# Kernel tuning notes

Measured on AMD Instinct MI355X. Metric: run time of the kernel, lower is better.

The kernel has to match this reference:

```python
import jax, jax.numpy as jnp
import numpy as np

B, C, H, W = 32, 3, 224, 224
P = 16
D = 768
HEADS, DH = 12, 64
INNER = HEADS * DH          # 768
DEPTH = 12
NUM_CLASSES = 1000
NP_ = (H // P) * (W // P)   # 196 patches
N = NP_ + 1                 # with cls token
PATCH_DIM = C * P * P       # 768
EPS = 1e-5


def _ln(x, g, b):
    mu = jnp.mean(x, axis=-1, keepdims=True)
    var = jnp.var(x, axis=-1, keepdims=True)
    return (x - mu) * jax.lax.rsqrt(var + EPS) * g + b


def setup_inputs() -> dict:
    key = jax.random.key(0)
    ks = jax.random.split(key, 16)
    s = 0.02
    return {
        "img": jax.random.normal(ks[0], (B, C, H, W), jnp.float32),
        "sph_dist": jax.random.uniform(ks[1], (N, N), jnp.float32),
        "patch_ln_g": jnp.ones((PATCH_DIM,), jnp.float32),
        "patch_ln_b": jnp.zeros((PATCH_DIM,), jnp.float32),
        "W_patch": jax.random.normal(ks[2], (PATCH_DIM, D), jnp.float32) * s,
        "b_patch": jnp.zeros((D,), jnp.float32),
        "emb_ln_g": jnp.ones((D,), jnp.float32),
        "emb_ln_b": jnp.zeros((D,), jnp.float32),
        "pos_emb": jax.random.normal(ks[3], (1, N, D), jnp.float32),
        "cls_tok": jax.random.normal(ks[4], (1, 1, D), jnp.float32),
        "ln_g": jnp.ones((DEPTH, D), jnp.float32),
        "ln_b": jnp.zeros((DEPTH, D), jnp.float32),
        "W_qkv": jax.random.normal(ks[5], (DEPTH, D, 3 * INNER), jnp.float32) * s,
        "W_out": jax.random.normal(ks[6], (DEPTH, INNER, D), jnp.float32) * s,
        "b_out": jnp.zeros((DEPTH, D), jnp.float32),
        "final_ln_g": jnp.ones((D,), jnp.float32),
        "final_ln_b": jnp.zeros((D,), jnp.float32),
        "W_head": jax.random.normal(ks[7], (D, NUM_CLASSES), jnp.float32) * s,
        "b_head": jnp.zeros((NUM_CLASSES,), jnp.float32),
    }


def _patchify(img):
    b = img.shape[0]
    # 'b c (h p1) (w p2) -> b (h w) (p1 p2 c)'
    x = img.reshape(b, C, H // P, P, W // P, P)
    x = x.transpose(0, 2, 4, 3, 5, 1)  # b h w p1 p2 c
    return x.reshape(b, NP_, PATCH_DIM)


def _attn_layer(x, sph_dist, g, bln, Wqkv, Wout, bout):
    b, n, _ = x.shape
    xn = _ln(x, g, bln)
    qkv = xn @ Wqkv                                  # [b,n,3*inner]
    q, k, v = jnp.split(qkv, 3, axis=-1)
    def heads(t):
        return t.reshape(b, n, HEADS, DH).transpose(0, 2, 1, 3)  # b h n d
    q, k, v = heads(q), heads(k), heads(v)
    dots = jnp.einsum('bhid,bhjd->bhij', q, k) * (DH ** -0.5)
    dw = dots * (1.0 + sph_dist)                     # broadcast over b,h
    mu = jnp.mean(dw, axis=1, keepdims=True)
    sd = jnp.std(dw, axis=1, keepdims=True, ddof=1)  # torch.std is unbiased
    dw = (dw - mu) / sd
    attn = jax.nn.softmax(dw, axis=-1)
    o = jnp.einsum('bhij,bhjd->bhid', attn, v)
    o = o.transpose(0, 2, 1, 3).reshape(b, n, INNER)
    return o @ Wout + bout


def reference(img, sph_dist, patch_ln_g, patch_ln_b, W_patch, b_patch,
              emb_ln_g, emb_ln_b, pos_emb, cls_tok,
              ln_g, ln_b, W_qkv, W_out, b_out,
              final_ln_g, final_ln_b, W_head, b_head):
    b = img.shape[0]
    x = _patchify(img)
    x = _ln(x, patch_ln_g, patch_ln_b)
    x = x @ W_patch + b_patch
    x = _ln(x, emb_ln_g, emb_ln_b)                   # [b, 196, D]
    cls = jnp.broadcast_to(cls_tok, (b, 1, D))
    x = jnp.concatenate([cls, x], axis=1)            # [b, 197, D]
    x = x + pos_emb[:, :x.shape[1]]
    for i in range(DEPTH):
        x = _attn_layer(x, sph_dist, ln_g[i], ln_b[i], W_qkv[i], W_out[i], b_out[i]) + x
    x = _ln(x, final_ln_g, final_ln_b)
    x = x[:, 0]                                      # cls pooling
    return x @ W_head + b_head
```

## Files before the change

### kernel.cpp

```cpp
#include <hip/hip_runtime.h>
#include <math.h>

constexpr int Bc = 32, Cch = 3, Hh = 224, Ww = 224, Pp = 16;
constexpr int Dd = 768, NH = 12, DHd = 64, INNERc = 768;
constexpr int DEPTHc = 12, NCLS = 1000;
constexpr int NPc = 196, Nn = 197, PD = 768;
constexpr float EPSf = 1e-5f;

typedef _Float16 half_t;
typedef __attribute__((ext_vector_type(8))) _Float16 half8;
typedef __attribute__((ext_vector_type(4))) float f32x4;
typedef __attribute__((ext_vector_type(4))) unsigned int uint32x4;

__device__ __forceinline__ float wave_red_sum(float v) {
#pragma unroll
    for (int m = 32; m; m >>= 1) v += __shfl_xor(v, m);
    return v;
}

__device__ __forceinline__ void block_red2(float& s, float& s2, float* red) {
    s = wave_red_sum(s);
    s2 = wave_red_sum(s2);
    int wid = threadIdx.x >> 6, lane = threadIdx.x & 63;
    if (lane == 0) { red[wid] = s; red[4 + wid] = s2; }
    __syncthreads();
    s = red[0] + red[1] + red[2] + red[3];
    s2 = red[4] + red[5] + red[6] + red[7];
}

__global__ __launch_bounds__(256) void k_patch_ln(
        const float* __restrict__ img, const float* __restrict__ g,
        const float* __restrict__ bb, half_t* __restrict__ out) {
    int pid = blockIdx.x;
    int b = pid / NPc, n = pid % NPc;
    int ph = n / 14, pw = n % 14;
    int t = threadIdx.x;
    __shared__ float red[8];
    float v[3];
#pragma unroll
    for (int i = 0; i < 3; i++) {
        int d = t + i * 256;
        int c = d % 3, q = (d / 3) & 15, p = d / 48;
        v[i] = img[((long)(b * Cch + c) * Hh + ph * Pp + p) * Ww + pw * Pp + q];
    }
    float s = v[0] + v[1] + v[2];
    float s2 = v[0] * v[0] + v[1] * v[1] + v[2] * v[2];
    block_red2(s, s2, red);
    float mu = s * (1.f / PD);
    float var = s2 * (1.f / PD) - mu * mu;
    float r = rsqrtf(var + EPSf);
#pragma unroll
    for (int i = 0; i < 3; i++) {
        int d = t + i * 256;
        out[(long)pid * PD + d] = (half_t)((v[i] - mu) * r * g[d] + bb[d]);
    }
}

template <typename T>
__global__ __launch_bounds__(256) void k_ln(
        const float* __restrict__ in, const float* __restrict__ g,
        const float* __restrict__ bb, T* __restrict__ out,
        long in_stride, long out_stride) {
    long row = blockIdx.x;
    const float* ip = in + row * in_stride;
    T* op = out + row * out_stride;
    int t = threadIdx.x;
    __shared__ float red[8];
    float v[3];
#pragma unroll
    for (int i = 0; i < 3; i++) v[i] = ip[t + i * 256];
    float s = v[0] + v[1] + v[2];
    float s2 = v[0] * v[0] + v[1] * v[1] + v[2] * v[2];
    block_red2(s, s2, red);
    float mu = s * (1.f / Dd);
    float var = s2 * (1.f / Dd) - mu * mu;
    float r = rsqrtf(var + EPSf);
#pragma unroll
    for (int i = 0; i < 3; i++) {
        int d = t + i * 256;
        op[d] = (T)((v[i] - mu) * r * g[d] + bb[d]);
    }
}

__global__ __launch_bounds__(256) void k_embed(
        const float* __restrict__ tmp, const float* __restrict__ cls,
        const float* __restrict__ pos, const float* __restrict__ g,
        const float* __restrict__ bb, float* __restrict__ x) {
    int pid = blockIdx.x;
    int b = pid / Nn, n = pid % Nn;
    int t = threadIdx.x;
    float* xp = x + (long)pid * Dd;
    if (n == 0) {
#pragma unroll
        for (int i = 0; i < 3; i++) {
            int d = t + i * 256;
            xp[d] = cls[d] + pos[d];
        }
        return;
    }
    const float* ip = tmp + (long)(b * NPc + n - 1) * Dd;
    __shared__ float red[8];
    float v[3];
#pragma unroll
    for (int i = 0; i < 3; i++) v[i] = ip[t + i * 256];
    float s = v[0] + v[1] + v[2];
    float s2 = v[0] * v[0] + v[1] * v[1] + v[2] * v[2];
    block_red2(s, s2, red);
    float mu = s * (1.f / Dd);
    float var = s2 * (1.f / Dd) - mu * mu;
    float r = rsqrtf(var + EPSf);
#pragma unroll
    for (int i = 0; i < 3; i++) {
        int d = t + i * 256;
        xp[d] = (v[i] - mu) * r * g[d] + bb[d] + pos[(long)n * Dd + d];
    }
}

__global__ __launch_bounds__(256) void k_wprep(
        const float* __restrict__ W, half_t* __restrict__ Wt, int K, int N) {
    W += (long)blockIdx.z * K * N;
    Wt += (long)blockIdx.z * K * N;
    __shared__ float tile[32][33];
    int n = blockIdx.x * 32 + threadIdx.x;
    int k0 = blockIdx.y * 32;
#pragma unroll
    for (int i = 0; i < 4; i++)
        tile[threadIdx.y + i * 8][threadIdx.x] = W[(long)(k0 + threadIdx.y + i * 8) * N + n];
    __syncthreads();
    int kk = k0 + threadIdx.x;
#pragma unroll
    for (int i = 0; i < 4; i++)
        Wt[(long)(blockIdx.x * 32 + threadIdx.y + i * 8) * K + kk] =
            (half_t)tile[threadIdx.x][threadIdx.y + i * 8];
}

__global__ __launch_bounds__(256) void k_wprep_head(
        const float* __restrict__ W, half_t* __restrict__ Wt) {
    __shared__ float tile[32][33];
    int n = blockIdx.x * 32 + threadIdx.x;
    int k0 = blockIdx.y * 32;
#pragma unroll
    for (int i = 0; i < 4; i++)
        tile[threadIdx.y + i * 8][threadIdx.x] =
            (n < NCLS) ? W[(long)(k0 + threadIdx.y + i * 8) * NCLS + n] : 0.f;
    __syncthreads();
    int kk = k0 + threadIdx.x;
#pragma unroll
    for (int i = 0; i < 4; i++)
        Wt[(long)(blockIdx.x * 32 + threadIdx.y + i * 8) * Dd + kk] =
            (half_t)tile[threadIdx.x][threadIdx.y + i * 8];
}

__global__ __launch_bounds__(256) void k_head(
        const half_t* __restrict__ Ah, const half_t* __restrict__ Wh,
        const float* __restrict__ bias, float* __restrict__ out) {
    int idx = blockIdx.x * 256 + threadIdx.x;
    int row = idx >> 10, col = idx & 1023;
    if (col >= NCLS) return;
    const half_t* ap = Ah + (long)row * Dd;
    const half_t* wp = Wh + (long)col * Dd;
    float acc = 0.f;
#pragma unroll
    for (int k = 0; k < 96; k++) {
        half8 a = *(const half8*)&ap[k * 8];
        half8 w = *(const half8*)&wp[k * 8];
#pragma unroll
        for (int u = 0; u < 8; u++) acc += (float)a[u] * (float)w[u];
    }
    out[(long)row * NCLS + col] = acc + bias[col];
}

__device__ __forceinline__ half8 lds_frag(const uint32x4 (*L)[8], int row, int slot) {
    union { uint32x4 u; half8 h; } t;
    t.u = L[row][slot];
    return t.h;
}

template <int HASB, int HASR, typename CT, int OMODE>
__global__ __launch_bounds__(256, 2) void k_hgemm(
        const half_t* __restrict__ A, const half_t* __restrict__ Bt,
        const float* __restrict__ bias, const float* __restrict__ res,
        CT* __restrict__ C, CT* __restrict__ C1, CT* __restrict__ C2,
        int M, int N, int K) {
    __shared__ uint32x4 smem[2176];
    uint32x4 (*As)[8] = (uint32x4(*)[8])smem;
    uint32x4 (*Bs)[8] = (uint32x4(*)[8])(smem + 1024);
    const int tid = threadIdx.x;
    const int nwg = gridDim.x;
    const int q8 = nwg >> 3, r8 = nwg & 7;
    const int xc = blockIdx.x & 7, oo = blockIdx.x >> 3;
    const int tile = (xc < r8 ? xc * (q8 + 1) : r8 * (q8 + 1) + (xc - r8) * q8) + oo;
    const int gx = N >> 7;
    const int n0 = (tile % gx) * 128, m0 = (tile / gx) * 128;
    const int lane = tid & 63, w = tid >> 6;
    const int wrr = (w >> 1) * 64, wcc = (w & 1) * 64;
    const int lrow = lane & 15, lgrp = lane >> 4;

    int lm[4], sw[4];
    long gA[4], gB[4];
    const int cb = (tid & 7) * 8;
#pragma unroll
    for (int c = 0; c < 4; ++c) {
        lm[c] = c * 32 + (tid >> 3);
        sw[c] = (tid & 7) ^ (lm[c] & 7);
        int ma = m0 + lm[c];
        if (ma > M - 1) ma = M - 1;
        gA[c] = (long)ma * K + cb;
        gB[c] = (long)(n0 + lm[c]) * K + cb;
    }

    f32x4 acc[4][4] = {};
    uint32x4 ra[4], rb[4];
#pragma unroll
    for (int c = 0; c < 4; ++c) { ra[c] = *(const uint32x4*)(A + gA[c]); rb[c] = *(const uint32x4*)(Bt + gB[c]); }
#pragma unroll
    for (int c = 0; c < 4; ++c) { As[lm[c]][sw[c]] = ra[c]; Bs[lm[c]][sw[c]] = rb[c]; }
    __syncthreads();

    const int nst = K >> 6;
    for (int t = 0; t < nst; ++t) {
        if (t + 1 < nst) {
            const int k0 = (t + 1) << 6;
#pragma unroll
            for (int c = 0; c < 4; ++c) {
                ra[c] = *(const uint32x4*)(A + gA[c] + k0);
                rb[c] = *(const uint32x4*)(Bt + gB[c] + k0);
            }
        }
#pragma unroll
        for (int kh = 0; kh < 2; ++kh) {
            half8 af[4], bf[4];
#pragma unroll
            for (int i2 = 0; i2 < 4; ++i2) {
                int m = wrr + i2 * 16 + lrow;
                af[i2] = lds_frag(As, m, (kh * 4 + lgrp) ^ (m & 7));
                int n = wcc + i2 * 16 + lrow;
                bf[i2] = lds_frag(Bs, n, (kh * 4 + lgrp) ^ (n & 7));
            }
#pragma unroll
            for (int i2 = 0; i2 < 4; ++i2)
#pragma unroll
                for (int j2 = 0; j2 < 4; ++j2)
                    acc[i2][j2] = __builtin_amdgcn_mfma_f32_16x16x32_f16(af[i2], bf[j2], acc[i2][j2], 0, 0, 0);
        }
        if (t + 1 < nst) {
            __syncthreads();
#pragma unroll
            for (int c = 0; c < 4; ++c) { As[lm[c]][sw[c]] = ra[c]; Bs[lm[c]][sw[c]] = rb[c]; }
            __syncthreads();
        }
    }

    if constexpr (sizeof(CT) == 2) {
        __syncthreads();
        half_t* Cs = (half_t*)smem;
#pragma unroll
        for (int i2 = 0; i2 < 4; ++i2)
#pragma unroll
            for (int j2 = 0; j2 < 4; ++j2) {
                int colc = wcc + j2 * 16 + lrow;
                float bv = HASB ? bias[n0 + colc] : 0.f;
#pragma unroll
                for (int q = 0; q < 4; ++q) {
                    int r = wrr + i2 * 16 + lgrp * 4 + q;
                    Cs[r * 136 + colc] = (half_t)(acc[i2][j2][q] + bv);
                }
            }
        __syncthreads();
#pragma unroll
        for (int it = 0; it < 8; ++it) {
            int idx = tid + it * 256;
            int row = idx >> 4, cu = idx & 15;
            int token = m0 + row;
            if (token < M) {
                uint32x4 val = *(const uint32x4*)(Cs + row * 136 + cu * 8);
                if constexpr (OMODE == 1) {
                    int gc = n0 + cu * 8;
                    int which = gc >= 1536 ? 2 : (gc >= 768 ? 1 : 0);
                    int rem = gc - which * 768;
                    int h = rem >> 6, d = rem & 63;
                    int b = token / Nn, nn = token - b * Nn;
                    CT* dst = (which == 0 ? C : which == 1 ? C1 : C2);
                    __builtin_nontemporal_store(val,
                        (uint32x4*)(dst + (((long)(b * NH + h) * Nn + nn) << 6) + d));
                } else {
                    __builtin_nontemporal_store(val,
                        (uint32x4*)(C + (long)token * N + n0 + cu * 8));
                }
            }
        }
    } else {
#pragma unroll
        for (int i2 = 0; i2 < 4; ++i2)
#pragma unroll
            for (int j2 = 0; j2 < 4; ++j2) {
                int colc = n0 + wcc + j2 * 16 + lrow;
                float bv = HASB ? bias[colc] : 0.f;
#pragma unroll
                for (int q = 0; q < 4; ++q) {
                    int r = m0 + wrr + i2 * 16 + lgrp * 4 + q;
                    if (r < M) {
                        float v = acc[i2][j2][q] + bv;
                        if (HASR) v += res[(long)r * N + colc];
                        __builtin_nontemporal_store(v, &C[(long)r * N + colc]);
                    }
                }
            }
    }
}

__global__ __launch_bounds__(256) void k_vtrans(
        const half_t* __restrict__ vh, half_t* __restrict__ vt) {
    const int bh = blockIdx.x;
    __shared__ half_t vsT[Nn][68];
    const int tid = threadIdx.x;
    const half_t* Vp = vh + (long)bh * Nn * 64;
    for (int idx = tid; idx < Nn * 8; idx += 256) {
        int r = idx >> 3, c8 = (idx & 7) * 8;
        *(half8*)&vsT[r][c8] = *(const half8*)&Vp[(long)r * 64 + c8];
    }
    __syncthreads();
    half_t* Tp = vt + (long)bh * 64 * 224;
    for (int idx = tid; idx < 64 * 112; idx += 256) {
        int d = idx / 112, p = idx % 112;
        int n0 = p * 2;
        union { unsigned int u; half_t h[2]; } t;
        t.h[0] = (n0 < Nn) ? vsT[n0][d] : (half_t)0.f;
        t.h[1] = (n0 + 1 < Nn) ? vsT[n0 + 1][d] : (half_t)0.f;
        *(unsigned int*)&Tp[(long)d * 224 + n0] = t.u;
    }
}

__global__ __launch_bounds__(256) void k_stats(
        const half_t* __restrict__ qh, const half_t* __restrict__ kh,
        f32x4* __restrict__ muT, f32x4* __restrict__ rsT) {
    const int blk = (blockIdx.x & 7) * 169 + (blockIdx.x >> 3);
    const int w = threadIdx.x >> 6, lane = threadIdx.x & 63;
    const int task = blk * 4 + w;
    const int b = task / 169, r = task % 169;
    const int it = r / 13, jt = r % 13;
    const int lrow = lane & 15, lg = lane >> 4;
    const int i0 = it * 16, j0 = jt * 16;
    const int arow = min(i0 + lrow, Nn - 1);
    const int jr = min(j0 + lrow, Nn - 1);
    const int hbase = b * NH;

    float sv[4] = {}, sq[4] = {};
#pragma unroll
    for (int h = 0; h < NH; h++) {
        const half_t* Qp = qh + ((long)(hbase + h) * Nn) * 64;
        const half_t* Kp = kh + ((long)(hbase + h) * Nn) * 64;
        half8 af0 = *(const half8*)&Qp[(long)arow * 64 + lg * 8];
        half8 af1 = *(const half8*)&Qp[(long)arow * 64 + 32 + lg * 8];
        half8 bf0 = *(const half8*)&Kp[(long)jr * 64 + lg * 8];
        half8 bf1 = *(const half8*)&Kp[(long)jr * 64 + 32 + lg * 8];
        f32x4 acc = {};
        acc = __builtin_amdgcn_mfma_f32_16x16x32_f16(af0, bf0, acc, 0, 0, 0);
        acc = __builtin_amdgcn_mfma_f32_16x16x32_f16(af1, bf1, acc, 0, 0, 0);
#pragma unroll
        for (int q = 0; q < 4; q++) { sv[q] += acc[q]; sq[q] += acc[q] * acc[q]; }
    }
    f32x4 muv, rsv;
#pragma unroll
    for (int q = 0; q < 4; q++) {
        float mu = sv[q] * (1.f / NH);
        float var = (sq[q] - sv[q] * mu) * (1.f / (NH - 1));
        muv[q] = mu;
        rsv[q] = rsqrtf(var);
    }
    long idx = ((long)(b * 13 + it) * 13 + jt) * 64 + lane;
    muT[idx] = muv;
    rsT[idx] = rsv;
}

__global__ __launch_bounds__(64) void k_attn2(
        const half_t* __restrict__ qh, const half_t* __restrict__ kh,
        const half_t* __restrict__ vt, const f32x4* __restrict__ muT,
        const f32x4* __restrict__ rsT, half_t* __restrict__ o) {
    __shared__ half_t PB[16][232];
    const int tile = (blockIdx.x & 7) * 624 + (blockIdx.x >> 3);
    const int bh = tile / 13, it = tile % 13;
    const int b = bh / NH, h = bh % NH;
    const int i0 = it * 16;
    const int lane = threadIdx.x;
    const int lrow = lane & 15, lg = lane >> 4;
    const int arow = min(i0 + lrow, Nn - 1);

    for (int idx = lane; idx < 16 * 12; idx += 64) {
        int rr = idx / 12, u = idx % 12;
        *(unsigned int*)&PB[rr][208 + u * 2] = 0u;
    }

    const half_t* Qp = qh + ((long)bh * Nn) * 64;
    const half_t* Kp = kh + ((long)bh * Nn) * 64;
    half8 af0 = *(const half8*)&Qp[(long)arow * 64 + lg * 8];
    half8 af1 = *(const half8*)&Qp[(long)arow * 64 + 32 + lg * 8];
    const f32x4* muB = muT + ((long)(b * 13 + it) * 13) * 64 + lane;
    const f32x4* rsB = rsT + ((long)(b * 13 + it) * 13) * 64 + lane;

    float ez[13][4];
    float mx[4] = {-1e30f, -1e30f, -1e30f, -1e30f};
#pragma unroll
    for (int jt = 0; jt < 13; jt++) {
        int jr = min(jt * 16 + lrow, Nn - 1);
        half8 bf0 = *(const half8*)&Kp[(long)jr * 64 + lg * 8];
        half8 bf1 = *(const half8*)&Kp[(long)jr * 64 + 32 + lg * 8];
        f32x4 acc = {};
        acc = __builtin_amdgcn_mfma_f32_16x16x32_f16(af0, bf0, acc, 0, 0, 0);
        acc = __builtin_amdgcn_mfma_f32_16x16x32_f16(af1, bf1, acc, 0, 0, 0);
        f32x4 mu4 = muB[jt * 64];
        f32x4 rs4 = rsB[jt * 64];
        bool joob = (jt * 16 + lrow) > Nn - 1;
#pragma unroll
        for (int q = 0; q < 4; q++) {
            float z = (acc[q] - mu4[q]) * rs4[q];
            if (joob) z = -1e30f;
            ez[jt][q] = z;
            mx[q] = fmaxf(mx[q], z);
        }
    }
#pragma unroll
    for (int st = 1; st <= 8; st <<= 1)
#pragma unroll
        for (int q = 0; q < 4; q++) mx[q] = fmaxf(mx[q], __shfl_xor(mx[q], st));
    float sm[4] = {0.f, 0.f, 0.f, 0.f};
#pragma unroll
    for (int jt = 0; jt < 13; jt++)
#pragma unroll
        for (int q = 0; q < 4; q++) {
            float e = __expf(ez[jt][q] - mx[q]);
            ez[jt][q] = e;
            sm[q] += e;
        }
#pragma unroll
    for (int st = 1; st <= 8; st <<= 1)
#pragma unroll
        for (int q = 0; q < 4; q++) sm[q] += __shfl_xor(sm[q], st);
    float inv[4];
#pragma unroll
    for (int q = 0; q < 4; q++) inv[q] = 1.f / sm[q];
#pragma unroll
    for (int jt = 0; jt < 13; jt++)
#pragma unroll
        for (int q = 0; q < 4; q++)
            PB[lg * 4 + q][jt * 16 + lrow] = (half_t)(ez[jt][q] * inv[q]);
    __syncthreads();

    const half_t* Vtp = vt + ((long)bh * 64) * 224;
#pragma unroll
    for (int dt = 0; dt < 4; dt++) {
        f32x4 oacc = {};
#pragma unroll
        for (int kt = 0; kt < 7; kt++) {
            half8 pa = *(const half8*)&PB[lrow][kt * 32 + lg * 8];
            half8 vb = *(const half8*)&Vtp[(long)(dt * 16 + lrow) * 224 + kt * 32 + lg * 8];
            oacc = __builtin_amdgcn_mfma_f32_16x16x32_f16(pa, vb, oacc, 0, 0, 0);
        }
#pragma unroll
        for (int q = 0; q < 4; q++) {
            int i = i0 + lg * 4 + q;
            if (i < Nn)
                o[((long)(b * Nn) + i) * INNERc + h * 64 + dt * 16 + lrow] = (half_t)oacc[q];
        }
    }
}

extern "C" void kernel_launch(void* const* d_in, const int* in_sizes, int n_in,
                              void* d_out, int out_size, void* d_ws, size_t ws_size,
                              hipStream_t stream) {
    const float* img     = (const float*)d_in[0];
    const float* patch_g = (const float*)d_in[2];
    const float* patch_b = (const float*)d_in[3];
    const float* W_patch = (const float*)d_in[4];
    const float* b_patch = (const float*)d_in[5];
    const float* emb_g   = (const float*)d_in[6];
    const float* emb_b   = (const float*)d_in[7];
    const float* pos     = (const float*)d_in[8];
    const float* cls     = (const float*)d_in[9];
    const float* ln_g    = (const float*)d_in[10];
    const float* ln_b    = (const float*)d_in[11];
    const float* W_qkv   = (const float*)d_in[12];
    const float* W_out   = (const float*)d_in[13];
    const float* b_out   = (const float*)d_in[14];
    const float* fin_g   = (const float*)d_in[15];
    const float* fin_b   = (const float*)d_in[16];
    const float* W_head  = (const float*)d_in[17];
    const float* b_head  = (const float*)d_in[18];
    float* out = (float*)d_out;

    const long SZ_XD  = (long)Bc * Nn * Dd;
    const long SZ_HD  = (long)Bc * NH * Nn * DHd;
    const long SZ_VT  = (long)Bc * NH * 64 * 224;
    const long SZ_TMP = (long)Bc * NPc * Dd;
    const long SZ_MU  = (long)Bc * 169 * 256 + 1024;

    float* x    = (float*)d_ws;
    float* tmp  = x + SZ_XD;
    float* muG  = tmp + SZ_TMP;
    float* rsG  = muG + SZ_MU;
    half_t* xh       = (half_t*)(rsG + SZ_MU);
    half_t* qhb      = xh + SZ_XD;
    half_t* khb      = qhb + SZ_HD;
    half_t* vhb      = khb + SZ_HD;
    half_t* vtb      = vhb + SZ_HD;
    half_t* clsh     = vtb + SZ_VT;
    half_t* wh_head  = clsh + 32 * Dd;
    half_t* wt_patch = wh_head + 1024 * Dd;
    half_t* wt_qkv   = wt_patch + (long)Dd * Dd;
    half_t* wt_out   = wt_qkv + (long)DEPTHc * 3 * INNERc * Dd;

    hipLaunchKernelGGL(k_wprep, dim3(Dd / 32, Dd / 32, 1), dim3(32, 8), 0, stream,
                       W_patch, wt_patch, Dd, Dd);
    hipLaunchKernelGGL(k_wprep, dim3(3 * INNERc / 32, Dd / 32, DEPTHc), dim3(32, 8), 0, stream,
                       W_qkv, wt_qkv, Dd, 3 * INNERc);
    hipLaunchKernelGGL(k_wprep, dim3(Dd / 32, Dd / 32, DEPTHc), dim3(32, 8), 0, stream,
                       W_out, wt_out, Dd, Dd);
    hipLaunchKernelGGL(k_wprep_head, dim3(32, 24), dim3(32, 8), 0, stream,
                       W_head, wh_head);

    hipLaunchKernelGGL(k_patch_ln, dim3(Bc * NPc), dim3(256), 0, stream,
                       img, patch_g, patch_b, xh);
    hipLaunchKernelGGL((k_hgemm<1, 0, float, 0>), dim3(6 * 49), dim3(256), 0, stream,
                       xh, wt_patch, b_patch, nullptr, tmp, nullptr, nullptr,
                       Bc * NPc, Dd, Dd);
    hipLaunchKernelGGL(k_embed, dim3(Bc * Nn), dim3(256), 0, stream,
                       tmp, cls, pos, emb_g, emb_b, x);

    const int Mrows = Bc * Nn;
    for (int l = 0; l < DEPTHc; l++) {
        const float* g  = ln_g + (long)l * Dd;
        const float* bb = ln_b + (long)l * Dd;
        const half_t* Wq = wt_qkv + (long)l * 3 * INNERc * Dd;
        const half_t* Wo = wt_out + (long)l * Dd * Dd;
        const float* bo = b_out + (long)l * Dd;
        hipLaunchKernelGGL((k_ln<half_t>), dim3(Mrows), dim3(256), 0, stream,
                           x, g, bb, xh, (long)Dd, (long)Dd);
        hipLaunchKernelGGL((k_hgemm<0, 0, half_t, 1>), dim3(18 * 50), dim3(256), 0, stream,
                           xh, Wq, nullptr, nullptr, qhb, khb, vhb,
                           Mrows, 3 * INNERc, Dd);
        hipLaunchKernelGGL(k_vtrans, dim3(Bc * NH), dim3(256), 0, stream,
                           vhb, vtb);
        hipLaunchKernelGGL(k_stats, dim3(1352), dim3(256), 0, stream,
                           qhb, khb, (f32x4*)muG, (f32x4*)rsG);
        hipLaunchKernelGGL(k_attn2, dim3(4992), dim3(64), 0, stream,
                           qhb, khb, vtb, (const f32x4*)muG, (const f32x4*)rsG, xh);
        hipLaunchKernelGGL((k_hgemm<1, 1, float, 0>), dim3(6 * 50), dim3(256), 0, stream,
                           xh, Wo, bo, x, x, nullptr, nullptr,
                           Mrows, Dd, Dd);
    }
    hipLaunchKernelGGL((k_ln<half_t>), dim3(Bc), dim3(256), 0, stream,
                       x, fin_g, fin_b, clsh, (long)Nn * Dd, (long)Dd);
    hipLaunchKernelGGL(k_head, dim3(128), dim3(256), 0, stream,
                       clsh, wh_head, b_head, out);
}
```

Measured before the change: 1.881 ms.

## Fuse pre-attention LayerNorm into QKV GEMM and write V transposed directly

The QKV GEMM now reads the fp32 residual stream directly. Each block computes per-row mean and rstd in a prologue and normalizes while packing A tiles to fp16, which removes the separate LN kernel and the fp16 activation round trip. V-column tiles are stored straight into the transposed V layout from the accumulators, so the k_vtrans kernel and its intermediate buffer go away. In exchange, every column tile recomputes the row statistics, A loads become fp32 (twice the bytes, 18x redundant across N tiles), and the V stores are scattered 2-byte writes. Variance is computed as E[x^2]-mu^2.

Result: slower. 3.245 ms (+72.5%).

```diff
diff --git a/kernel.cpp b/kernel.cpp
--- a/kernel.cpp
+++ b/kernel.cpp
@@ -170,21 +170,38 @@
     out[(long)row * NCLS + col] = acc + bias[col];
 }
 
+__device__ __forceinline__ uint32x4 ln_pack(const float* xp, float mu, float rs,
+                                            f32x4 g0, f32x4 g1, f32x4 b0, f32x4 b1) {
+    f32x4 v0 = *(const f32x4*)xp;
+    f32x4 v1 = *(const f32x4*)(xp + 4);
+    union { uint32x4 u; half8 h; } t;
+#pragma unroll
+    for (int u2 = 0; u2 < 4; u2++) {
+        t.h[u2]     = (half_t)((v0[u2] - mu) * rs * g0[u2] + b0[u2]);
+        t.h[u2 + 4] = (half_t)((v1[u2] - mu) * rs * g1[u2] + b1[u2]);
+    }
+    return t.u;
+}
+
 __device__ __forceinline__ half8 lds_frag(const uint32x4 (*L)[8], int row, int slot) {
     union { uint32x4 u; half8 h; } t;
     t.u = L[row][slot];
     return t.h;
 }
 
-template <int HASB, int HASR, typename CT, int OMODE>
+template <int HASB, int HASR, typename CT, int OMODE, int LNF>
 __global__ __launch_bounds__(256, 2) void k_hgemm(
-        const half_t* __restrict__ A, const half_t* __restrict__ Bt,
+        const void* __restrict__ Av, const half_t* __restrict__ Bt,
         const float* __restrict__ bias, const float* __restrict__ res,
-        CT* __restrict__ C, CT* __restrict__ C1, CT* __restrict__ C2,
+        const float* __restrict__ lng, const float* __restrict__ lnb,
+        CT* __restrict__ C, CT* __restrict__ C1, half_t* __restrict__ Vt,
         int M, int N, int K) {
     __shared__ uint32x4 smem[2176];
+    __shared__ float murs[128][2];
     uint32x4 (*As)[8] = (uint32x4(*)[8])smem;
     uint32x4 (*Bs)[8] = (uint32x4(*)[8])(smem + 1024);
+    const half_t* Ah = (const half_t*)Av;
+    const float*  Af = (const float*)Av;
     const int tid = threadIdx.x;
     const int nwg = gridDim.x;
     const int q8 = nwg >> 3, r8 = nwg & 7;
@@ -196,6 +213,30 @@
     const int wrr = (w >> 1) * 64, wcc = (w & 1) * 64;
     const int lrow = lane & 15, lgrp = lane >> 4;
 
+    if constexpr (LNF) {
+        int rowp = tid >> 1, hf = tid & 1;
+        const float* xr = Af + (long)min(m0 + rowp, M - 1) * K + hf * (K / 2);
+        float s = 0.f, s2 = 0.f;
+        for (int k = 0; k < K / 2; k += 8) {
+            f32x4 v0 = *(const f32x4*)(xr + k);
+            f32x4 v1 = *(const f32x4*)(xr + k + 4);
+#pragma unroll
+            for (int u = 0; u < 4; u++) {
+                s += v0[u] + v1[u];
+                s2 += v0[u] * v0[u] + v1[u] * v1[u];
+            }
+        }
+        s += __shfl_xor(s, 1);
+        s2 += __shfl_xor(s2, 1);
+        if (hf == 0) {
+            float mu = s * (1.f / K);
+            float var = s2 * (1.f / K) - mu * mu;
+            murs[rowp][0] = mu;
+            murs[rowp][1] = rsqrtf(var + EPSf);
+        }
+        __syncthreads();
+    }
+
     int lm[4], sw[4];
     long gA[4], gB[4];
     const int cb = (tid & 7) * 8;
@@ -208,22 +249,45 @@
         gA[c] = (long)ma * K + cb;
         gB[c] = (long)(n0 + lm[c]) * K + cb;
     }
+    float muc[4], rsc[4];
+    if constexpr (LNF) {
+#pragma unroll
+        for (int c = 0; c < 4; ++c) { muc[c] = murs[lm[c]][0]; rsc[c] = murs[lm[c]][1]; }
+    }
 
     f32x4 acc[4][4] = {};
-    uint32x4 ra[4], rb[4];
-#pragma unroll
-    for (int c = 0; c < 4; ++c) { ra[c] = *(const uint32x4*)(A + gA[c]); rb[c] = *(const uint32x4*)(Bt + gB[c]); }
-#pragma unroll
-    for (int c = 0; c < 4; ++c) { As[lm[c]][sw[c]] = ra[c]; Bs[lm[c]][sw[c]] = rb[c]; }
+    uint32x4 ha[4], rb[4];
+    f32x4 gv0, gv1, bv0, bv1;
+    if constexpr (LNF) {
+        gv0 = *(const f32x4*)(lng + cb);  gv1 = *(const f32x4*)(lng + cb + 4);
+        bv0 = *(const f32x4*)(lnb + cb);  bv1 = *(const f32x4*)(lnb + cb + 4);
+    }
+#pragma unroll
+    for (int c = 0; c < 4; ++c) {
+        if constexpr (LNF)
+            ha[c] = ln_pack(Af + gA[c], muc[c], rsc[c], gv0, gv1, bv0, bv1);
+        else
+            ha[c] = *(const uint32x4*)(Ah + gA[c]);
+        rb[c] = *(const uint32x4*)(Bt + gB[c]);
+    }
+#pragma unroll
+    for (int c = 0; c < 4; ++c) { As[lm[c]][sw[c]] = ha[c]; Bs[lm[c]][sw[c]] = rb[c]; }
     __syncthreads();
 
     const int nst = K >> 6;
     for (int t = 0; t < nst; ++t) {
         if (t + 1 < nst) {
             const int k0 = (t + 1) << 6;
+            if constexpr (LNF) {
+                gv0 = *(const f32x4*)(lng + k0 + cb);  gv1 = *(const f32x4*)(lng + k0 + cb + 4);
+                bv0 = *(const f32x4*)(lnb + k0 + cb);  bv1 = *(const f32x4*)(lnb + k0 + cb + 4);
+            }
 #pragma unroll
             for (int c = 0; c < 4; ++c) {
-                ra[c] = *(const uint32x4*)(A + gA[c] + k0);
+                if constexpr (LNF)
+                    ha[c] = ln_pack(Af + gA[c] + k0, muc[c], rsc[c], gv0, gv1, bv0, bv1);
+                else
+                    ha[c] = *(const uint32x4*)(Ah + gA[c] + k0);
                 rb[c] = *(const uint32x4*)(Bt + gB[c] + k0);
             }
         }
@@ -246,12 +310,34 @@
         if (t + 1 < nst) {
             __syncthreads();
 #pragma unroll
-            for (int c = 0; c < 4; ++c) { As[lm[c]][sw[c]] = ra[c]; Bs[lm[c]][sw[c]] = rb[c]; }
+            for (int c = 0; c < 4; ++c) { As[lm[c]][sw[c]] = ha[c]; Bs[lm[c]][sw[c]] = rb[c]; }
             __syncthreads();
         }
     }
 
     if constexpr (sizeof(CT) == 2) {
+        if constexpr (OMODE == 1) {
+            if (n0 >= 1536) {
+#pragma unroll
+                for (int i2 = 0; i2 < 4; ++i2)
+#pragma unroll
+                    for (int j2 = 0; j2 < 4; ++j2) {
+                        int colc = wcc + j2 * 16 + lrow;
+                        int rem = n0 + colc - 1536;
+                        int h = rem >> 6, d = rem & 63;
+#pragma unroll
+                        for (int q = 0; q < 4; ++q) {
+                            int token = m0 + wrr + i2 * 16 + lgrp * 4 + q;
+                            if (token < M) {
+                                int b = token / Nn, nn = token - b * Nn;
+                                __builtin_nontemporal_store((half_t)acc[i2][j2][q],
+                                    Vt + ((long)(b * NH + h) * 64 + d) * 224 + nn);
+                            }
+                        }
+                    }
+                return;
+            }
+        }
         __syncthreads();
         half_t* Cs = (half_t*)smem;
 #pragma unroll
@@ -276,11 +362,11 @@
                 uint32x4 val = *(const uint32x4*)(Cs + row * 136 + cu * 8);
                 if constexpr (OMODE == 1) {
                     int gc = n0 + cu * 8;
-                    int which = gc >= 1536 ? 2 : (gc >= 768 ? 1 : 0);
+                    int which = gc >= 768 ? 1 : 0;
                     int rem = gc - which * 768;
                     int h = rem >> 6, d = rem & 63;
                     int b = token / Nn, nn = token - b * Nn;
-                    CT* dst = (which == 0 ? C : which == 1 ? C1 : C2);
+                    CT* dst = (which == 0 ? C : C1);
                     __builtin_nontemporal_store(val,
                         (uint32x4*)(dst + (((long)(b * NH + h) * Nn + nn) << 6) + d));
                 } else {
@@ -306,28 +392,6 @@
                     }
                 }
             }
-    }
-}
-
-__global__ __launch_bounds__(256) void k_vtrans(
-        const half_t* __restrict__ vh, half_t* __restrict__ vt) {
-    const int bh = blockIdx.x;
-    __shared__ half_t vsT[Nn][68];
-    const int tid = threadIdx.x;
-    const half_t* Vp = vh + (long)bh * Nn * 64;
-    for (int idx = tid; idx < Nn * 8; idx += 256) {
-        int r = idx >> 3, c8 = (idx & 7) * 8;
-        *(half8*)&vsT[r][c8] = *(const half8*)&Vp[(long)r * 64 + c8];
-    }
-    __syncthreads();
-    half_t* Tp = vt + (long)bh * 64 * 224;
-    for (int idx = tid; idx < 64 * 112; idx += 256) {
-        int d = idx / 112, p = idx % 112;
-        int n0 = p * 2;
-        union { unsigned int u; half_t h[2]; } t;
-        t.h[0] = (n0 < Nn) ? vsT[n0][d] : (half_t)0.f;
-        t.h[1] = (n0 + 1 < Nn) ? vsT[n0 + 1][d] : (half_t)0.f;
-        *(unsigned int*)&Tp[(long)d * 224 + n0] = t.u;
     }
 }
 
@@ -501,8 +565,7 @@
     half_t* xh       = (half_t*)(rsG + SZ_MU);
     half_t* qhb      = xh + SZ_XD;
     half_t* khb      = qhb + SZ_HD;
-    half_t* vhb      = khb + SZ_HD;
-    half_t* vtb      = vhb + SZ_HD;
+    half_t* vtb      = khb + SZ_HD;
     half_t* clsh     = vtb + SZ_VT;
     half_t* wh_head  = clsh + 32 * Dd;
     half_t* wt_patch = wh_head + 1024 * Dd;
@@ -520,9 +583,9 @@
 
     hipLaunchKernelGGL(k_patch_ln, dim3(Bc * NPc), dim3(256), 0, stream,
                        img, patch_g, patch_b, xh);
-    hipLaunchKernelGGL((k_hgemm<1, 0, float, 0>), dim3(6 * 49), dim3(256), 0, stream,
-                       xh, wt_patch, b_patch, nullptr, tmp, nullptr, nullptr,
-                       Bc * NPc, Dd, Dd);
+    hipLaunchKernelGGL((k_hgemm<1, 0, float, 0, 0>), dim3(6 * 49), dim3(256), 0, stream,
+                       xh, wt_patch, b_patch, nullptr, nullptr, nullptr,
+                       tmp, nullptr, nullptr, Bc * NPc, Dd, Dd);
     hipLaunchKernelGGL(k_embed, dim3(Bc * Nn), dim3(256), 0, stream,
                        tmp, cls, pos, emb_g, emb_b, x);
 
@@ -533,20 +596,16 @@
         const half_t* Wq = wt_qkv + (long)l * 3 * INNERc * Dd;
         const half_t* Wo = wt_out + (long)l * Dd * Dd;
         const float* bo = b_out + (long)l * Dd;
-        hipLaunchKernelGGL((k_ln<half_t>), dim3(Mrows), dim3(256), 0, stream,
-                           x, g, bb, xh, (long)Dd, (long)Dd);
-        hipLaunchKernelGGL((k_hgemm<0, 0, half_t, 1>), dim3(18 * 50), dim3(256), 0, stream,
-                           xh, Wq, nullptr, nullptr, qhb, khb, vhb,
-                           Mrows, 3 * INNERc, Dd);
-        hipLaunchKernelGGL(k_vtrans, dim3(Bc * NH), dim3(256), 0, stream,
-                           vhb, vtb);
+        hipLaunchKernelGGL((k_hgemm<0, 0, half_t, 1, 1>), dim3(18 * 50), dim3(256), 0, stream,
+                           x, Wq, nullptr, nullptr, g, bb,
+                           qhb, khb, vtb, Mrows, 3 * INNERc, Dd);
         hipLaunchKernelGGL(k_stats, dim3(1352), dim3(256), 0, stream,
                            qhb, khb, (f32x4*)muG, (f32x4*)rsG);
         hipLaunchKernelGGL(k_attn2, dim3(4992), dim3(64), 0, stream,
                            qhb, khb, vtb, (const f32x4*)muG, (const f32x4*)rsG, xh);
-        hipLaunchKernelGGL((k_hgemm<1, 1, float, 0>), dim3(6 * 50), dim3(256), 0, stream,
-                           xh, Wo, bo, x, x, nullptr, nullptr,
-                           Mrows, Dd, Dd);
+        hipLaunchKernelGGL((k_hgemm<1, 1, float, 0, 0>), dim3(6 * 50), dim3(256), 0, stream,
+                           xh, Wo, bo, x, nullptr, nullptr,
+                           x, nullptr, nullptr, Mrows, Dd, Dd);
     }
     hipLaunchKernelGGL((k_ln<half_t>), dim3(Bc), dim3(256), 0, stream,
                        x, fin_g, fin_b, clsh, (long)Nn * Dd, (long)Dd);
```
